# Optimization experiments

Measured on AMD Instinct MI355X. Metric: run time of the kernel, lower is better.

Reference implementation:

```python
import math
import jax, jax.numpy as jnp
import numpy as np

B, L, D = 8, 4096, 1024
H = 8
DK = D // H          # d_keys = d_values = 128
K_FACTOR = 2


def setup_inputs() -> dict:
    key = jax.random.key(0)
    ks = jax.random.split(key, 11)
    s = 0.02
    return {
        "queries": jax.random.normal(ks[0], (B, L, D), dtype=jnp.float32),
        "keys":    jax.random.normal(ks[1], (B, L, D), dtype=jnp.float32),
        "values":  jax.random.normal(ks[2], (B, L, D), dtype=jnp.float32),
        "Wq": jax.random.normal(ks[3], (D, H * DK), dtype=jnp.float32) * s,
        "bq": jnp.zeros((H * DK,), dtype=jnp.float32),
        "Wk": jax.random.normal(ks[4], (D, H * DK), dtype=jnp.float32) * s,
        "bk": jnp.zeros((H * DK,), dtype=jnp.float32),
        "Wv": jax.random.normal(ks[5], (D, H * DK), dtype=jnp.float32) * s,
        "bv": jnp.zeros((H * DK,), dtype=jnp.float32),
        "Wo": jax.random.normal(ks[6], (H * DK, D), dtype=jnp.float32) * s,
        "bo": jnp.zeros((D,), dtype=jnp.float32),
    }


def reference(queries, keys, values, Wq, bq, Wk, bk, Wv, bv, Wo, bo):
    b, l, _ = queries.shape
    # projections + head split: [B, L, H, DK]
    q = (queries @ Wq + bq).reshape(b, l, H, DK)
    k = (keys @ Wk + bk).reshape(b, l, H, DK)
    v = (values @ Wv + bv).reshape(b, l, H, DK)
    # L == S so the pad/truncate branch is a no-op (keys[:, :L] == keys)

    qT = q.transpose(0, 2, 3, 1)  # [B, H, DK, L]
    kT = k.transpose(0, 2, 3, 1)
    vT = v.transpose(0, 2, 3, 1)

    # FFT-based circular cross-correlation along time axis
    q_fft = jnp.fft.rfft(qT, axis=-1)
    k_fft = jnp.fft.rfft(kT, axis=-1)
    corr = jnp.fft.irfft(q_fft * jnp.conj(k_fft), n=l, axis=-1)  # [B, H, DK, L]

    # time-delay aggregation over top-k delays
    top_k = int(K_FACTOR * math.log(l))
    weights, delay = jax.lax.top_k(corr, top_k)        # [B, H, DK, K]
    tmp_corr = jax.nn.softmax(weights, axis=-1)
    tmp_values = jnp.concatenate([vT, vT], axis=-1)    # [B, H, DK, 2L] circular wrap
    init_index = jnp.arange(l)

    delay_k = jnp.moveaxis(delay, -1, 0)               # [K, B, H, DK]
    corr_k = jnp.moveaxis(tmp_corr, -1, 0)             # [K, B, H, DK]

    def step(acc, dc):
        d_i, c_i = dc                                  # [B, H, DK]
        idx = init_index[None, None, None, :] + d_i[..., None]   # [B, H, DK, L]
        pattern = jnp.take_along_axis(tmp_values, idx, axis=-1)
        return acc + pattern * c_i[..., None], None

    agg, _ = jax.lax.scan(step, jnp.zeros_like(vT), (delay_k, corr_k))

    out = agg.transpose(0, 3, 1, 2).reshape(b, l, H * DK)  # [B, L, H*DK]
    return out @ Wo + bo
```

## Files before the change

### kernel.cpp

```cpp
#include <hip/hip_runtime.h>
#include <hip/hip_bf16.h>
#include <string.h>

#define NB 8
#define LSEQ 4096
#define DMOD 1024
#define NCH (NB * DMOD)
#define TOPK 16

typedef unsigned short u16;
typedef unsigned int u32;
typedef __attribute__((ext_vector_type(4))) float f32x4;
typedef __attribute__((ext_vector_type(8))) _Float16 f16x8;

__device__ __forceinline__ float h2f(u16 u) {
  _Float16 h;
  __builtin_memcpy(&h, &u, 2);
  return (float)h;
}
__device__ __forceinline__ u16 f2h(float f) {
  _Float16 h = (_Float16)f;
  u16 u;
  __builtin_memcpy(&u, &h, 2);
  return u;
}
__device__ __forceinline__ u32 pk2(float a, float b) {
  return (u32)f2h(a) | ((u32)f2h(b) << 16);
}

__global__ __launch_bounds__(256) void twiddle_k(float2* tw) {
  int i = blockIdx.x * 256 + threadIdx.x;
  if (i < 2048) {
    float ang = -2.0f * 3.14159265358979323846f * (float)i / 4096.0f;
    tw[i] = make_float2(cosf(ang), sinf(ang));
  }
}

__global__ __launch_bounds__(256) void transpose_w_k(const float* __restrict__ src,
                                                     u16* __restrict__ dst,
                                                     int R, int C) {
  __shared__ u16 tile[64][66];
  int c0 = blockIdx.x * 64, r0 = blockIdx.y * 64;
  int tx = threadIdx.x & 63, ty = threadIdx.x >> 6;
#pragma unroll
  for (int i = 0; i < 16; i++) {
    int r = ty + i * 4;
    tile[r][tx] = f2h(src[(size_t)(r0 + r) * C + c0 + tx]);
  }
  __syncthreads();
#pragma unroll
  for (int i = 0; i < 16; i++) {
    int cc = ty + i * 4;
    dst[(size_t)(c0 + cc) * R + r0 + tx] = tile[tx][cc];
  }
}

__global__ __launch_bounds__(256) void gemm_proj_k(const float* __restrict__ A,
                                                   const u16* __restrict__ Btw,
                                                   const float* __restrict__ bias,
                                                   u16* __restrict__ out,
                                                   int K) {
  __shared__ __align__(16) u16 smem[17408];
  u16* As = smem;
  u16* Bs = smem + 5120;
  int tid = threadIdx.x;
  int lane = tid & 63, wave = tid >> 6;
  int quad = lane >> 4, l15 = lane & 15;
  int m0 = blockIdx.y * 128, n0 = blockIdx.x * 128;
  int wm = (wave >> 1) * 64, wn = (wave & 1) * 64;
  int r_a = tid >> 2, kc = (tid & 3) * 8;

  f32x4 acc[4][4];
#pragma unroll
  for (int i = 0; i < 4; i++)
#pragma unroll
    for (int j = 0; j < 4; j++)
      acc[i][j] = (f32x4){0.f, 0.f, 0.f, 0.f};

  for (int kk = 0; kk < K; kk += 32) {
    __syncthreads();
    const float* ga0 = A + (size_t)(m0 + r_a) * K + kk + kc;
    const float* ga1 = ga0 + (size_t)64 * K;
    float4 x0 = *(const float4*)ga0;
    float4 x1 = *(const float4*)(ga0 + 4);
    float4 y0 = *(const float4*)ga1;
    float4 y1 = *(const float4*)(ga1 + 4);
    uint4 wa, wb;
    wa.x = pk2(x0.x, x0.y); wa.y = pk2(x0.z, x0.w);
    wa.z = pk2(x1.x, x1.y); wa.w = pk2(x1.z, x1.w);
    wb.x = pk2(y0.x, y0.y); wb.y = pk2(y0.z, y0.w);
    wb.z = pk2(y1.x, y1.y); wb.w = pk2(y1.z, y1.w);
    *(uint4*)&As[r_a * 40 + kc] = wa;
    *(uint4*)&As[(r_a + 64) * 40 + kc] = wb;
    const u16* gb = Btw + (size_t)(n0 + r_a) * K + kk + kc;
    *(uint4*)&Bs[r_a * 40 + kc] = *(const uint4*)gb;
    *(uint4*)&Bs[(r_a + 64) * 40 + kc] = *(const uint4*)(gb + (size_t)64 * K);
    __syncthreads();
    f16x8 af[4], bfr[4];
    int ka = quad * 8;
#pragma unroll
    for (int i = 0; i < 4; i++)
      af[i] = *(const f16x8*)&As[(wm + i * 16 + l15) * 40 + ka];
#pragma unroll
    for (int j = 0; j < 4; j++)
      bfr[j] = *(const f16x8*)&Bs[(wn + j * 16 + l15) * 40 + ka];
#pragma unroll
    for (int i = 0; i < 4; i++)
#pragma unroll
      for (int j = 0; j < 4; j++)
        acc[i][j] = __builtin_amdgcn_mfma_f32_16x16x32_f16(af[i], bfr[j], acc[i][j], 0, 0, 0);
  }

  __syncthreads();
  float bv[4];
#pragma unroll
  for (int j = 0; j < 4; j++) bv[j] = bias[n0 + wn + j * 16 + l15];
  u16* Ct = smem;
#pragma unroll
  for (int i = 0; i < 4; i++) {
#pragma unroll
    for (int j = 0; j < 4; j++) {
      int ml = wm + i * 16 + quad * 4;
      int nl = wn + j * 16 + l15;
      unsigned long long pkv = 0;
#pragma unroll
      for (int r = 0; r < 4; r++)
        pkv |= ((unsigned long long)f2h(acc[i][j][r] + bv[j])) << (16 * r);
      *(unsigned long long*)&Ct[nl * 136 + ml] = pkv;
    }
  }
  __syncthreads();
  int b_ = m0 >> 12, t0 = m0 & 4095;
#pragma unroll
  for (int it = 0; it < 8; it++) {
    int row = (tid >> 4) + it * 16;
    int col = (tid & 15) * 8;
    uint4 v = *(const uint4*)&Ct[row * 136 + col];
    *(uint4*)(out + (size_t)b_ * DMOD * LSEQ + (size_t)(n0 + row) * LSEQ + t0 + col) = v;
  }
}

__global__ __launch_bounds__(256) void gemm_tA_k(const u16* __restrict__ Acm,
                                                 const u16* __restrict__ Wot,
                                                 const float* __restrict__ bias,
                                                 float* __restrict__ out) {
  __shared__ __align__(16) u16 smem[17408];
  u32* Ta = (u32*)smem;
  u16* Bs = smem + 4224;
  int tid = threadIdx.x;
  int lane = tid & 63, wave = tid >> 6;
  int quad = lane >> 4, l15 = lane & 15;
  int b = blockIdx.z;
  int m0 = blockIdx.y * 128, n0 = blockIdx.x * 128;
  int wm = (wave >> 1) * 64, wn = (wave & 1) * 64;
  int cp = tid >> 4, t0s = (tid & 15) * 8;
  int r_b = tid >> 2, kc = (tid & 3) * 8;
  const u16* Ab = Acm + (size_t)b * DMOD * LSEQ;

  f32x4 acc[4][4];
#pragma unroll
  for (int i = 0; i < 4; i++)
#pragma unroll
    for (int j = 0; j < 4; j++)
      acc[i][j] = (f32x4){0.f, 0.f, 0.f, 0.f};

  for (int kk = 0; kk < DMOD; kk += 32) {
    __syncthreads();
    const u16* ga = Ab + (size_t)(kk + 2 * cp) * LSEQ + m0 + t0s;
    uint4 v0 = *(const uint4*)ga;
    uint4 v1 = *(const uint4*)(ga + LSEQ);
    int tb = cp * 132 + t0s;
    uint4 w0, w1;
    w0.x = (v0.x & 0xffffu) | (v1.x << 16);
    w0.y = (v0.x >> 16) | (v1.x & 0xffff0000u);
    w0.z = (v0.y & 0xffffu) | (v1.y << 16);
    w0.w = (v0.y >> 16) | (v1.y & 0xffff0000u);
    w1.x = (v0.z & 0xffffu) | (v1.z << 16);
    w1.y = (v0.z >> 16) | (v1.z & 0xffff0000u);
    w1.z = (v0.w & 0xffffu) | (v1.w << 16);
    w1.w = (v0.w >> 16) | (v1.w & 0xffff0000u);
    *(uint4*)&Ta[tb] = w0;
    *(uint4*)&Ta[tb + 4] = w1;
    const u16* gb = Wot + (size_t)(n0 + r_b) * DMOD + kk + kc;
    *(uint4*)&Bs[r_b * 40 + kc] = *(const uint4*)gb;
    *(uint4*)&Bs[(r_b + 64) * 40 + kc] = *(const uint4*)(gb + (size_t)64 * DMOD);
    __syncthreads();
    f16x8 af[4], bfr[4];
    int ka = quad * 8;
#pragma unroll
    for (int i = 0; i < 4; i++) {
      int mrow = wm + i * 16 + l15;
      uint4 fa;
      fa.x = Ta[(quad * 4 + 0) * 132 + mrow];
      fa.y = Ta[(quad * 4 + 1) * 132 + mrow];
      fa.z = Ta[(quad * 4 + 2) * 132 + mrow];
      fa.w = Ta[(quad * 4 + 3) * 132 + mrow];
      af[i] = *(f16x8*)&fa;
    }
#pragma unroll
    for (int j = 0; j < 4; j++)
      bfr[j] = *(const f16x8*)&Bs[(wn + j * 16 + l15) * 40 + ka];
#pragma unroll
    for (int i = 0; i < 4; i++)
#pragma unroll
      for (int j = 0; j < 4; j++)
        acc[i][j] = __builtin_amdgcn_mfma_f32_16x16x32_f16(af[i], bfr[j], acc[i][j], 0, 0, 0);
  }

  float bv[4];
#pragma unroll
  for (int j = 0; j < 4; j++) bv[j] = bias[n0 + wn + j * 16 + l15];
  float* Cf = (float*)smem;
#pragma unroll
  for (int half = 0; half < 2; half++) {
    __syncthreads();
    if ((wave >> 1) == half) {
#pragma unroll
      for (int i = 0; i < 4; i++) {
#pragma unroll
        for (int j = 0; j < 4; j++) {
          int mlocal = i * 16 + quad * 4;
          int nl = wn + j * 16 + l15;
#pragma unroll
          for (int r = 0; r < 4; r++)
            Cf[(mlocal + r) * 132 + nl] = acc[i][j][r] + bv[j];
        }
      }
    }
    __syncthreads();
#pragma unroll
    for (int it = 0; it < 8; it++) {
      int row = (tid >> 5) + it * 8;
      int col = (tid & 31) * 4;
      float4 v = *(const float4*)&Cf[row * 132 + col];
      *(float4*)(out + (size_t)b * LSEQ * DMOD +
                 (size_t)(m0 + half * 64 + row) * DMOD + n0 + col) = v;
    }
  }
}

__global__ __launch_bounds__(256) void fft_corr_topk_k(const u16* __restrict__ Qt,
                                                       const u16* __restrict__ Kt,
                                                       const float2* __restrict__ tw,
                                                       float* __restrict__ topw,
                                                       int* __restrict__ topd) {
  __shared__ float2 buf[2][4096];
  int ch = blockIdx.x;
  int tid = threadIdx.x;
  const u16* qrow = Qt + (size_t)ch * LSEQ;
  const u16* krow = Kt + (size_t)ch * LSEQ;
#pragma unroll
  for (int p = 0; p < 16; p++) {
    int idx = tid + p * 256;
    buf[0][idx] = make_float2(h2f(qrow[idx]), h2f(krow[idx]));
  }
  int srcb = 0, m = 1;
#pragma unroll
  for (int s = 0; s < 12; s++) {
    __syncthreads();
    const float2* src = buf[srcb];
    float2* dst = buf[srcb ^ 1];
#pragma unroll
    for (int p = 0; p < 8; p++) {
      int idx = tid + p * 256;
      int k = idx & (m - 1);
      int jm = idx - k;
      float2 c0 = src[idx];
      float2 c1 = src[idx + 2048];
      float2 w = tw[jm];
      dst[idx + jm] = make_float2(c0.x + c1.x, c0.y + c1.y);
      float2 d = make_float2(c0.x - c1.x, c0.y - c1.y);
      dst[idx + jm + m] = make_float2(d.x * w.x - d.y * w.y, d.x * w.y + d.y * w.x);
    }
    srcb ^= 1;
    m <<= 1;
  }
  __syncthreads();
#pragma unroll
  for (int p = 0; p < 16; p++) {
    int f = tid + p * 256;
    float2 zf = buf[0][f];
    float2 zn = buf[0][(4096 - f) & 4095];
    float2 zc = make_float2(zn.x, -zn.y);
    float2 a = make_float2(zf.x + zc.x, zf.y + zc.y);
    float2 d = make_float2(zf.x - zc.x, zf.y - zc.y);
    float2 dc = make_float2(d.x, -d.y);
    float px = a.x * dc.x - a.y * dc.y;
    float py = a.x * dc.y + a.y * dc.x;
    buf[1][f] = make_float2(-0.25f * py, 0.25f * px);
  }
  srcb = 1; m = 1;
#pragma unroll
  for (int s = 0; s < 12; s++) {
    __syncthreads();
    const float2* src = buf[srcb];
    float2* dst = buf[srcb ^ 1];
#pragma unroll
    for (int p = 0; p < 8; p++) {
      int idx = tid + p * 256;
      int k = idx & (m - 1);
      int jm = idx - k;
      float2 c0 = src[idx];
      float2 c1 = src[idx + 2048];
      float2 w = tw[jm];
      w.y = -w.y;
      dst[idx + jm] = make_float2(c0.x + c1.x, c0.y + c1.y);
      float2 d = make_float2(c0.x - c1.x, c0.y - c1.y);
      dst[idx + jm + m] = make_float2(d.x * w.x - d.y * w.y, d.x * w.y + d.y * w.x);
    }
    srcb ^= 1;
    m <<= 1;
  }
  __syncthreads();
  float* scr = (float*)buf[0];
  float* tv = scr + 8;
  int* tdl = (int*)(scr + 24);
  const float NEGINF = -__builtin_inff();
  for (int r = 0; r < TOPK; r++) {
    float bvv = NEGINF;
    int bi = 0;
    for (int p = 0; p < 16; p++) {
      int t = tid + p * 256;
      float v = buf[1][t].x;
      if (v > bvv) { bvv = v; bi = t; }
    }
#pragma unroll
    for (int off = 32; off > 0; off >>= 1) {
      float ov = __shfl_down(bvv, off);
      int oi = __shfl_down(bi, off);
      if (ov > bvv || (ov == bvv && oi < bi)) { bvv = ov; bi = oi; }
    }
    if ((tid & 63) == 0) { scr[tid >> 6] = bvv; ((int*)scr)[4 + (tid >> 6)] = bi; }
    __syncthreads();
    if (tid == 0) {
      float fb = scr[0]; int fi = ((int*)scr)[4];
      for (int wv = 1; wv < 4; wv++) {
        float ov = scr[wv]; int oi = ((int*)scr)[4 + wv];
        if (ov > fb || (ov == fb && oi < fi)) { fb = ov; fi = oi; }
      }
      tv[r] = fb; tdl[r] = fi;
      buf[1][fi].x = NEGINF;
    }
    __syncthreads();
  }
  if (tid == 0) {
    float mx = tv[0];
    float e[TOPK];
    float s = 0.f;
    for (int k2 = 0; k2 < TOPK; k2++) {
      e[k2] = __expf((tv[k2] - mx) * (1.0f / 4096.0f));
      s += e[k2];
    }
    float inv = 1.0f / s;
    for (int k2 = 0; k2 < TOPK; k2++) {
      topw[(size_t)ch * TOPK + k2] = e[k2] * inv;
      topd[(size_t)ch * TOPK + k2] = tdl[k2];
    }
  }
}

__global__ __launch_bounds__(256) void aggregate_k(const u16* __restrict__ Vt,
                                                   const float* __restrict__ topw,
                                                   const int* __restrict__ topd,
                                                   u16* __restrict__ agg) {
  __shared__ u16 vrow[4096];
  __shared__ float w_s[TOPK];
  __shared__ int d_s[TOPK];
  int ch = blockIdx.x, tid = threadIdx.x;
  const u16* src = Vt + (size_t)ch * LSEQ;
#pragma unroll
  for (int p = 0; p < 16; p++) vrow[tid + p * 256] = src[tid + p * 256];
  if (tid < TOPK) {
    w_s[tid] = topw[(size_t)ch * TOPK + tid];
    d_s[tid] = topd[(size_t)ch * TOPK + tid];
  }
  __syncthreads();
#pragma unroll
  for (int p = 0; p < 16; p++) {
    int t = tid + p * 256;
    float s = 0.f;
#pragma unroll
    for (int k = 0; k < TOPK; k++)
      s += w_s[k] * h2f(vrow[(t + d_s[k]) & 4095]);
    agg[(size_t)ch * LSEQ + t] = f2h(s);
  }
}

extern "C" void kernel_launch(void* const* d_in, const int* in_sizes, int n_in,
                              void* d_out, int out_size, void* d_ws, size_t ws_size,
                              hipStream_t stream) {
  (void)in_sizes; (void)n_in; (void)out_size; (void)ws_size;
  const float* queries = (const float*)d_in[0];
  const float* keys    = (const float*)d_in[1];
  const float* values  = (const float*)d_in[2];
  const float* Wq = (const float*)d_in[3];
  const float* bq = (const float*)d_in[4];
  const float* Wk = (const float*)d_in[5];
  const float* bk = (const float*)d_in[6];
  const float* Wv = (const float*)d_in[7];
  const float* bv = (const float*)d_in[8];
  const float* Wo = (const float*)d_in[9];
  const float* bo = (const float*)d_in[10];

  char* ws = (char*)d_ws;
  u16* ws0 = (u16*)ws;
  u16* Wqt = (u16*)(ws + (64ull << 20));
  u16* Wkt = Wqt + 1024 * 1024;
  u16* Wvt = Wkt + 1024 * 1024;
  u16* Wot = Wvt + 1024 * 1024;
  float2* tw = (float2*)(ws + (72ull << 20));
  float* topw = (float*)(ws + (72ull << 20) + (64ull << 10));
  int* topd = (int*)(ws + (72ull << 20) + (64ull << 10) + (512ull << 10));

  u16* Qt = ws0;
  u16* Kt = (u16*)d_out;
  u16* Vt = (u16*)d_out;
  u16* agg = ws0;

  twiddle_k<<<dim3(8), dim3(256), 0, stream>>>(tw);
  transpose_w_k<<<dim3(16, 16), dim3(256), 0, stream>>>(Wq, Wqt, 1024, 1024);
  transpose_w_k<<<dim3(16, 16), dim3(256), 0, stream>>>(Wk, Wkt, 1024, 1024);
  transpose_w_k<<<dim3(16, 16), dim3(256), 0, stream>>>(Wv, Wvt, 1024, 1024);
  transpose_w_k<<<dim3(16, 16), dim3(256), 0, stream>>>(Wo, Wot, 1024, 1024);
  dim3 gg(8, 256);
  gemm_proj_k<<<gg, dim3(256), 0, stream>>>(queries, Wqt, bq, Qt, 1024);
  gemm_proj_k<<<gg, dim3(256), 0, stream>>>(keys, Wkt, bk, Kt, 1024);
  fft_corr_topk_k<<<dim3(NCH), dim3(256), 0, stream>>>(Qt, Kt, tw, topw, topd);
  gemm_proj_k<<<gg, dim3(256), 0, stream>>>(values, Wvt, bv, Vt, 1024);
  aggregate_k<<<dim3(NCH), dim3(256), 0, stream>>>(Vt, topw, topd, agg);
  gemm_tA_k<<<dim3(8, 32, 8), dim3(256), 0, stream>>>(agg, Wot, bo, (float*)d_out);
}
```

Baseline: 1.588 ms.

## Replace radix-2 Stockham FFT with register radix-16 FFT and incremental top-k

The FFT correlation kernel now runs a three-pass radix-16 decomposition in registers, with swizzled shared-memory exchanges between passes. This replaces 12 radix-2 stages per transform, each with its own barrier and double-buffered shared memory. The twiddle table grows to the full 4096 entries, shared memory drops to a single buffer, and launch bounds ask for 4 blocks per CU. Top-k keeps a per-thread maximum candidate that only the winning thread recomputes each round, instead of rescanning all 4096 values every round. This adds register pressure and more complex indexing.

Measured after the change: 1.461 ms. -8.0%, faster.

```diff
diff --git a/kernel.cpp b/kernel.cpp
--- a/kernel.cpp
+++ b/kernel.cpp
@@ -27,10 +27,16 @@
 __device__ __forceinline__ u32 pk2(float a, float b) {
   return (u32)f2h(a) | ((u32)f2h(b) << 16);
 }
+__device__ __forceinline__ float2 cmul(float2 a, float2 b) {
+  return make_float2(a.x * b.x - a.y * b.y, a.x * b.y + a.y * b.x);
+}
+__device__ __forceinline__ float2 cmul_conj(float2 a, float2 b) {
+  return make_float2(a.x * b.x + a.y * b.y, a.y * b.x - a.x * b.y);
+}
 
 __global__ __launch_bounds__(256) void twiddle_k(float2* tw) {
   int i = blockIdx.x * 256 + threadIdx.x;
-  if (i < 2048) {
+  if (i < 4096) {
     float ang = -2.0f * 3.14159265358979323846f * (float)i / 4096.0f;
     tw[i] = make_float2(cosf(ang), sinf(ang));
   }
@@ -239,122 +245,214 @@
   }
 }
 
-__global__ __launch_bounds__(256) void fft_corr_topk_k(const u16* __restrict__ Qt,
-                                                       const u16* __restrict__ Kt,
-                                                       const float2* __restrict__ tw,
-                                                       float* __restrict__ topw,
-                                                       int* __restrict__ topd) {
-  __shared__ float2 buf[2][4096];
+#define SWZ(t) ((t) ^ (((t) >> 4) & 15))
+
+template <bool INV>
+__device__ __forceinline__ void dft16(float2* z) {
+  const float SQ = 0.70710678118654752440f;
+  const float C1 = 0.92387953251128675613f;
+  const float S1 = 0.38268343236508977173f;
+  const float sg = INV ? 1.0f : -1.0f;
+#pragma unroll
+  for (int i = 0; i < 16; i += 2) {
+    float2 a = z[i], b = z[i + 1];
+    z[i] = make_float2(a.x + b.x, a.y + b.y);
+    z[i + 1] = make_float2(a.x - b.x, a.y - b.y);
+  }
+  {
+    const float wre[2] = {1.f, 0.f};
+    const float wim[2] = {0.f, sg};
+#pragma unroll
+    for (int g = 0; g < 16; g += 4)
+#pragma unroll
+      for (int p = 0; p < 2; p++) {
+        float2 a = z[g + p], b = z[g + p + 2];
+        float2 t = make_float2(b.x * wre[p] - b.y * wim[p],
+                               b.x * wim[p] + b.y * wre[p]);
+        z[g + p] = make_float2(a.x + t.x, a.y + t.y);
+        z[g + p + 2] = make_float2(a.x - t.x, a.y - t.y);
+      }
+  }
+  {
+    const float wre[4] = {1.f, SQ, 0.f, -SQ};
+    const float wim[4] = {0.f, sg * SQ, sg, sg * SQ};
+#pragma unroll
+    for (int g = 0; g < 16; g += 8)
+#pragma unroll
+      for (int p = 0; p < 4; p++) {
+        float2 a = z[g + p], b = z[g + p + 4];
+        float2 t = make_float2(b.x * wre[p] - b.y * wim[p],
+                               b.x * wim[p] + b.y * wre[p]);
+        z[g + p] = make_float2(a.x + t.x, a.y + t.y);
+        z[g + p + 4] = make_float2(a.x - t.x, a.y - t.y);
+      }
+  }
+  {
+    const float wre[8] = {1.f, C1, SQ, S1, 0.f, -S1, -SQ, -C1};
+    const float wim[8] = {0.f, sg * S1, sg * SQ, sg * C1, sg, sg * C1, sg * SQ, sg * S1};
+#pragma unroll
+    for (int p = 0; p < 8; p++) {
+      float2 a = z[p], b = z[p + 8];
+      float2 t = make_float2(b.x * wre[p] - b.y * wim[p],
+                             b.x * wim[p] + b.y * wre[p]);
+      z[p] = make_float2(a.x + t.x, a.y + t.y);
+      z[p + 8] = make_float2(a.x - t.x, a.y - t.y);
+    }
+  }
+}
+
+__global__ __launch_bounds__(256, 4) void fft_corr_topk_k(const u16* __restrict__ Qt,
+                                                          const u16* __restrict__ Kt,
+                                                          const float2* __restrict__ tw,
+                                                          float* __restrict__ topw,
+                                                          int* __restrict__ topd) {
+  __shared__ float2 buf[4096];
+  __shared__ float candv[256];
+  __shared__ int candi[256];
+  __shared__ float tvs[TOPK];
+  __shared__ int tds[TOPK];
+  __shared__ int winner;
   int ch = blockIdx.x;
   int tid = threadIdx.x;
   const u16* qrow = Qt + (size_t)ch * LSEQ;
   const u16* krow = Kt + (size_t)ch * LSEQ;
-#pragma unroll
-  for (int p = 0; p < 16; p++) {
-    int idx = tid + p * 256;
-    buf[0][idx] = make_float2(h2f(qrow[idx]), h2f(krow[idx]));
-  }
-  int srcb = 0, m = 1;
-#pragma unroll
-  for (int s = 0; s < 12; s++) {
-    __syncthreads();
-    const float2* src = buf[srcb];
-    float2* dst = buf[srcb ^ 1];
-#pragma unroll
-    for (int p = 0; p < 8; p++) {
-      int idx = tid + p * 256;
-      int k = idx & (m - 1);
-      int jm = idx - k;
-      float2 c0 = src[idx];
-      float2 c1 = src[idx + 2048];
-      float2 w = tw[jm];
-      dst[idx + jm] = make_float2(c0.x + c1.x, c0.y + c1.y);
-      float2 d = make_float2(c0.x - c1.x, c0.y - c1.y);
-      dst[idx + jm + m] = make_float2(d.x * w.x - d.y * w.y, d.x * w.y + d.y * w.x);
-    }
-    srcb ^= 1;
-    m <<= 1;
-  }
-  __syncthreads();
-#pragma unroll
-  for (int p = 0; p < 16; p++) {
-    int f = tid + p * 256;
-    float2 zf = buf[0][f];
-    float2 zn = buf[0][(4096 - f) & 4095];
-    float2 zc = make_float2(zn.x, -zn.y);
-    float2 a = make_float2(zf.x + zc.x, zf.y + zc.y);
-    float2 d = make_float2(zf.x - zc.x, zf.y - zc.y);
-    float2 dc = make_float2(d.x, -d.y);
-    float px = a.x * dc.x - a.y * dc.y;
-    float py = a.x * dc.y + a.y * dc.x;
-    buf[1][f] = make_float2(-0.25f * py, 0.25f * px);
-  }
-  srcb = 1; m = 1;
-#pragma unroll
-  for (int s = 0; s < 12; s++) {
-    __syncthreads();
-    const float2* src = buf[srcb];
-    float2* dst = buf[srcb ^ 1];
-#pragma unroll
-    for (int p = 0; p < 8; p++) {
-      int idx = tid + p * 256;
-      int k = idx & (m - 1);
-      int jm = idx - k;
-      float2 c0 = src[idx];
-      float2 c1 = src[idx + 2048];
-      float2 w = tw[jm];
-      w.y = -w.y;
-      dst[idx + jm] = make_float2(c0.x + c1.x, c0.y + c1.y);
-      float2 d = make_float2(c0.x - c1.x, c0.y - c1.y);
-      dst[idx + jm + m] = make_float2(d.x * w.x - d.y * w.y, d.x * w.y + d.y * w.x);
-    }
-    srcb ^= 1;
-    m <<= 1;
-  }
-  __syncthreads();
-  float* scr = (float*)buf[0];
-  float* tv = scr + 8;
-  int* tdl = (int*)(scr + 24);
+  const int rev[16] = {0, 8, 4, 12, 2, 10, 6, 14, 1, 9, 5, 13, 3, 11, 7, 15};
+  float2 z[16];
+
+#pragma unroll
+  for (int r = 0; r < 16; r++) {
+    int t = tid + 256 * r;
+    z[rev[r]] = make_float2(h2f(qrow[t]), h2f(krow[t]));
+  }
+  dft16<false>(z);
+#pragma unroll
+  for (int u = 0; u < 16; u++) {
+    float2 w = tw[(u * tid) & 4095];
+    buf[SWZ(16 * tid + u)] = cmul(z[u], w);
+  }
+  __syncthreads();
+
+  {
+    int k16 = tid & 15, j = tid >> 4;
+#pragma unroll
+    for (int r = 0; r < 16; r++) z[rev[r]] = buf[SWZ(tid + 256 * r)];
+    __syncthreads();
+    dft16<false>(z);
+#pragma unroll
+    for (int u = 0; u < 16; u++) {
+      float2 w = tw[(u * j * 16) & 4095];
+      buf[SWZ(256 * j + k16 + 16 * u)] = cmul(z[u], w);
+    }
+  }
+  __syncthreads();
+
+#pragma unroll
+  for (int r = 0; r < 16; r++) z[rev[r]] = buf[SWZ(tid + 256 * r)];
+  __syncthreads();
+  dft16<false>(z);
+#pragma unroll
+  for (int u = 0; u < 16; u++) buf[SWZ(tid + 256 * u)] = z[u];
+  __syncthreads();
+
+#pragma unroll
+  for (int r = 0; r < 16; r++) {
+    int t = tid + 256 * r;
+    float2 zf = buf[SWZ(t)];
+    float2 zn = buf[SWZ((4096 - t) & 4095)];
+    float ax = zf.x + zn.x, ay = zf.y - zn.y;
+    float dx = zf.x - zn.x, dy = zf.y + zn.y;
+    float px = ax * dx + ay * dy;
+    float py = ay * dx - ax * dy;
+    z[rev[r]] = make_float2(-0.25f * py, 0.25f * px);
+  }
+  __syncthreads();
+  dft16<true>(z);
+#pragma unroll
+  for (int u = 0; u < 16; u++) {
+    float2 w = tw[(u * tid) & 4095];
+    buf[SWZ(16 * tid + u)] = cmul_conj(z[u], w);
+  }
+  __syncthreads();
+
+  {
+    int k16 = tid & 15, j = tid >> 4;
+#pragma unroll
+    for (int r = 0; r < 16; r++) z[rev[r]] = buf[SWZ(tid + 256 * r)];
+    __syncthreads();
+    dft16<true>(z);
+#pragma unroll
+    for (int u = 0; u < 16; u++) {
+      float2 w = tw[(u * j * 16) & 4095];
+      buf[SWZ(256 * j + k16 + 16 * u)] = cmul_conj(z[u], w);
+    }
+  }
+  __syncthreads();
+
+#pragma unroll
+  for (int r = 0; r < 16; r++) z[rev[r]] = buf[SWZ(tid + 256 * r)];
+  dft16<true>(z);
+  float vals[16];
+#pragma unroll
+  for (int u = 0; u < 16; u++) vals[u] = z[u].x;
+
   const float NEGINF = -__builtin_inff();
+  {
+    float bvv = vals[0];
+    int bu = 0;
+#pragma unroll
+    for (int u = 1; u < 16; u++)
+      if (vals[u] > bvv) { bvv = vals[u]; bu = u; }
+    candv[tid] = bvv;
+    candi[tid] = tid + (bu << 8);
+  }
   for (int r = 0; r < TOPK; r++) {
-    float bvv = NEGINF;
-    int bi = 0;
-    for (int p = 0; p < 16; p++) {
-      int t = tid + p * 256;
-      float v = buf[1][t].x;
-      if (v > bvv) { bvv = v; bi = t; }
-    }
-#pragma unroll
-    for (int off = 32; off > 0; off >>= 1) {
-      float ov = __shfl_down(bvv, off);
-      int oi = __shfl_down(bi, off);
-      if (ov > bvv || (ov == bvv && oi < bi)) { bvv = ov; bi = oi; }
-    }
-    if ((tid & 63) == 0) { scr[tid >> 6] = bvv; ((int*)scr)[4 + (tid >> 6)] = bi; }
-    __syncthreads();
-    if (tid == 0) {
-      float fb = scr[0]; int fi = ((int*)scr)[4];
-      for (int wv = 1; wv < 4; wv++) {
-        float ov = scr[wv]; int oi = ((int*)scr)[4 + wv];
-        if (ov > fb || (ov == fb && oi < fi)) { fb = ov; fi = oi; }
+    __syncthreads();
+    if (tid < 64) {
+      float v0 = candv[tid];
+      int i0 = candi[tid];
+#pragma unroll
+      for (int s2 = 1; s2 < 4; s2++) {
+        float v1 = candv[tid + 64 * s2];
+        int i1 = candi[tid + 64 * s2];
+        if (v1 > v0 || (v1 == v0 && i1 < i0)) { v0 = v1; i0 = i1; }
       }
-      tv[r] = fb; tdl[r] = fi;
-      buf[1][fi].x = NEGINF;
-    }
-    __syncthreads();
-  }
+#pragma unroll
+      for (int off = 32; off > 0; off >>= 1) {
+        float ov = __shfl_down(v0, off);
+        int oi = __shfl_down(i0, off);
+        if (ov > v0 || (ov == v0 && oi < i0)) { v0 = ov; i0 = oi; }
+      }
+      if (tid == 0) { tvs[r] = v0; tds[r] = i0; winner = i0; }
+    }
+    __syncthreads();
+    int wn = winner;
+    if ((wn & 255) == tid) {
+      int ku = wn >> 8;
+#pragma unroll
+      for (int u = 0; u < 16; u++)
+        if (u == ku) vals[u] = NEGINF;
+      float bvv = vals[0];
+      int bu = 0;
+#pragma unroll
+      for (int u = 1; u < 16; u++)
+        if (vals[u] > bvv) { bvv = vals[u]; bu = u; }
+      candv[tid] = bvv;
+      candi[tid] = tid + (bu << 8);
+    }
+  }
+  __syncthreads();
   if (tid == 0) {
-    float mx = tv[0];
+    float mx = tvs[0];
     float e[TOPK];
     float s = 0.f;
     for (int k2 = 0; k2 < TOPK; k2++) {
-      e[k2] = __expf((tv[k2] - mx) * (1.0f / 4096.0f));
+      e[k2] = __expf((tvs[k2] - mx) * (1.0f / 4096.0f));
       s += e[k2];
     }
     float inv = 1.0f / s;
     for (int k2 = 0; k2 < TOPK; k2++) {
       topw[(size_t)ch * TOPK + k2] = e[k2] * inv;
-      topd[(size_t)ch * TOPK + k2] = tdl[k2];
+      topd[(size_t)ch * TOPK + k2] = tds[k2];
     }
   }
 }
@@ -417,7 +515,7 @@
   u16* Vt = (u16*)d_out;
   u16* agg = ws0;
 
-  twiddle_k<<<dim3(8), dim3(256), 0, stream>>>(tw);
+  twiddle_k<<<dim3(16), dim3(256), 0, stream>>>(tw);
   transpose_w_k<<<dim3(16, 16), dim3(256), 0, stream>>>(Wq, Wqt, 1024, 1024);
   transpose_w_k<<<dim3(16, 16), dim3(256), 0, stream>>>(Wk, Wkt, 1024, 1024);
   transpose_w_k<<<dim3(16, 16), dim3(256), 0, stream>>>(Wv, Wvt, 1024, 1024);
```

## Rewrite FFT correlation as register radix-16 passes with swizzled LDS and incremental top-k

Applied to the files above, without the earlier changes.

Replaces the 12-stage radix-2 Stockham FFT, which did two shared-memory round trips per stage, with a three-pass radix-16 decomposition held in registers. Twiddles are applied between passes and shared memory is XOR-swizzled to avoid bank conflicts. Shared memory drops to one buffer, and launch bounds request four blocks per CU. Top-k selection now keeps a per-thread candidate list and rescans only the winning thread's 16 values each round, instead of rescanning all 4096 with a full block reduction. The twiddle table grows to 4096 entries, and the higher register count per thread may limit occupancy.

Result: faster. 1.439 ms (-9.4%).

```diff
diff --git a/kernel.cpp b/kernel.cpp
--- a/kernel.cpp
+++ b/kernel.cpp
@@ -27,10 +27,16 @@
 __device__ __forceinline__ u32 pk2(float a, float b) {
   return (u32)f2h(a) | ((u32)f2h(b) << 16);
 }
+__device__ __forceinline__ float2 cmul(float2 a, float2 b) {
+  return make_float2(a.x * b.x - a.y * b.y, a.x * b.y + a.y * b.x);
+}
+__device__ __forceinline__ float2 cmul_conj(float2 a, float2 b) {
+  return make_float2(a.x * b.x + a.y * b.y, a.y * b.x - a.x * b.y);
+}
 
 __global__ __launch_bounds__(256) void twiddle_k(float2* tw) {
   int i = blockIdx.x * 256 + threadIdx.x;
-  if (i < 2048) {
+  if (i < 4096) {
     float ang = -2.0f * 3.14159265358979323846f * (float)i / 4096.0f;
     tw[i] = make_float2(cosf(ang), sinf(ang));
   }
@@ -239,122 +245,167 @@
   }
 }
 
-__global__ __launch_bounds__(256) void fft_corr_topk_k(const u16* __restrict__ Qt,
-                                                       const u16* __restrict__ Kt,
-                                                       const float2* __restrict__ tw,
-                                                       float* __restrict__ topw,
-                                                       int* __restrict__ topd) {
-  __shared__ float2 buf[2][4096];
+#define SWZ(t) ((t) ^ (((t) >> 4) & 15))
+
+#define FOREACH16(M) M(0) M(1) M(2) M(3) M(4) M(5) M(6) M(7) \
+                     M(8) M(9) M(10) M(11) M(12) M(13) M(14) M(15)
+#define BITREV16(M) M(0,0) M(1,8) M(2,4) M(3,12) M(4,2) M(5,10) M(6,6) M(7,14) \
+                    M(8,1) M(9,9) M(10,5) M(11,13) M(12,3) M(13,11) M(14,7) M(15,15)
+
+#define BF(a, b) { float tx = (b).x, ty = (b).y; \
+                   (b).x = (a).x - tx; (b).y = (a).y - ty; \
+                   (a).x += tx; (a).y += ty; }
+#define BFW(a, b, wr, wi) { float tx = (b).x*(wr) - (b).y*(wi); \
+                            float ty = (b).x*(wi) + (b).y*(wr); \
+                            (b).x = (a).x - tx; (b).y = (a).y - ty; \
+                            (a).x += tx; (a).y += ty; }
+
+#define FFT_SQ 0.70710678118654752440f
+#define FFT_C1 0.92387953251128675613f
+#define FFT_S1 0.38268343236508977173f
+
+#define DFT16(SGc) \
+  BF(z0,z1) BF(z2,z3) BF(z4,z5) BF(z6,z7) BF(z8,z9) BF(z10,z11) BF(z12,z13) BF(z14,z15) \
+  BF(z0,z2) BFW(z1,z3,0.f,(SGc)) BF(z4,z6) BFW(z5,z7,0.f,(SGc)) \
+  BF(z8,z10) BFW(z9,z11,0.f,(SGc)) BF(z12,z14) BFW(z13,z15,0.f,(SGc)) \
+  BF(z0,z4) BFW(z1,z5,FFT_SQ,(SGc)*FFT_SQ) BFW(z2,z6,0.f,(SGc)) BFW(z3,z7,-FFT_SQ,(SGc)*FFT_SQ) \
+  BF(z8,z12) BFW(z9,z13,FFT_SQ,(SGc)*FFT_SQ) BFW(z10,z14,0.f,(SGc)) BFW(z11,z15,-FFT_SQ,(SGc)*FFT_SQ) \
+  BF(z0,z8) BFW(z1,z9,FFT_C1,(SGc)*FFT_S1) BFW(z2,z10,FFT_SQ,(SGc)*FFT_SQ) BFW(z3,z11,FFT_S1,(SGc)*FFT_C1) \
+  BFW(z4,z12,0.f,(SGc)) BFW(z5,z13,-FFT_S1,(SGc)*FFT_C1) BFW(z6,z14,-FFT_SQ,(SGc)*FFT_SQ) BFW(z7,z15,-FFT_C1,(SGc)*FFT_S1)
+
+__global__ __launch_bounds__(256, 4)
+void fft_corr_topk_k(const u16* __restrict__ Qt,
+                     const u16* __restrict__ Kt,
+                     const float2* __restrict__ tw,
+                     float* __restrict__ topw,
+                     int* __restrict__ topd) {
+  __shared__ float2 buf[4096];
+  __shared__ float candv[256];
+  __shared__ int candi[256];
+  __shared__ float tvs[TOPK];
+  __shared__ int tds[TOPK];
+  __shared__ int winner;
   int ch = blockIdx.x;
   int tid = threadIdx.x;
   const u16* qrow = Qt + (size_t)ch * LSEQ;
   const u16* krow = Kt + (size_t)ch * LSEQ;
-#pragma unroll
-  for (int p = 0; p < 16; p++) {
-    int idx = tid + p * 256;
-    buf[0][idx] = make_float2(h2f(qrow[idx]), h2f(krow[idx]));
-  }
-  int srcb = 0, m = 1;
-#pragma unroll
-  for (int s = 0; s < 12; s++) {
-    __syncthreads();
-    const float2* src = buf[srcb];
-    float2* dst = buf[srcb ^ 1];
-#pragma unroll
-    for (int p = 0; p < 8; p++) {
-      int idx = tid + p * 256;
-      int k = idx & (m - 1);
-      int jm = idx - k;
-      float2 c0 = src[idx];
-      float2 c1 = src[idx + 2048];
-      float2 w = tw[jm];
-      dst[idx + jm] = make_float2(c0.x + c1.x, c0.y + c1.y);
-      float2 d = make_float2(c0.x - c1.x, c0.y - c1.y);
-      dst[idx + jm + m] = make_float2(d.x * w.x - d.y * w.y, d.x * w.y + d.y * w.x);
-    }
-    srcb ^= 1;
-    m <<= 1;
-  }
-  __syncthreads();
-#pragma unroll
-  for (int p = 0; p < 16; p++) {
-    int f = tid + p * 256;
-    float2 zf = buf[0][f];
-    float2 zn = buf[0][(4096 - f) & 4095];
-    float2 zc = make_float2(zn.x, -zn.y);
-    float2 a = make_float2(zf.x + zc.x, zf.y + zc.y);
-    float2 d = make_float2(zf.x - zc.x, zf.y - zc.y);
-    float2 dc = make_float2(d.x, -d.y);
-    float px = a.x * dc.x - a.y * dc.y;
-    float py = a.x * dc.y + a.y * dc.x;
-    buf[1][f] = make_float2(-0.25f * py, 0.25f * px);
-  }
-  srcb = 1; m = 1;
-#pragma unroll
-  for (int s = 0; s < 12; s++) {
-    __syncthreads();
-    const float2* src = buf[srcb];
-    float2* dst = buf[srcb ^ 1];
-#pragma unroll
-    for (int p = 0; p < 8; p++) {
-      int idx = tid + p * 256;
-      int k = idx & (m - 1);
-      int jm = idx - k;
-      float2 c0 = src[idx];
-      float2 c1 = src[idx + 2048];
-      float2 w = tw[jm];
-      w.y = -w.y;
-      dst[idx + jm] = make_float2(c0.x + c1.x, c0.y + c1.y);
-      float2 d = make_float2(c0.x - c1.x, c0.y - c1.y);
-      dst[idx + jm + m] = make_float2(d.x * w.x - d.y * w.y, d.x * w.y + d.y * w.x);
-    }
-    srcb ^= 1;
-    m <<= 1;
-  }
-  __syncthreads();
-  float* scr = (float*)buf[0];
-  float* tv = scr + 8;
-  int* tdl = (int*)(scr + 24);
+  const int jj = tid >> 4, k16 = tid & 15;
+
+#define DECLZ(u) float2 z##u;
+  FOREACH16(DECLZ)
+
+#define LD1(r, k) { int t = tid + 256 * (r); \
+                    z##k = make_float2(h2f(qrow[t]), h2f(krow[t])); }
+  BITREV16(LD1)
+  DFT16(-1.f)
+#define ST1(u) { float2 w = tw[((u) * tid) & 4095]; \
+                 buf[SWZ(16 * tid + (u))] = cmul(z##u, w); }
+  FOREACH16(ST1)
+  __syncthreads();
+
+#define LD2(r, k) z##k = buf[SWZ(tid + 256 * (r))];
+  BITREV16(LD2)
+  __syncthreads();
+  DFT16(-1.f)
+#define ST2F(u) { float2 w = tw[((u) * jj * 16) & 4095]; \
+                  buf[SWZ(256 * jj + k16 + 16 * (u))] = cmul(z##u, w); }
+  FOREACH16(ST2F)
+  __syncthreads();
+
+  BITREV16(LD2)
+  __syncthreads();
+  DFT16(-1.f)
+#define ST3(u) buf[SWZ(tid + 256 * (u))] = z##u;
+  FOREACH16(ST3)
+  __syncthreads();
+
+#define LDP(r, k) { int t = tid + 256 * (r); \
+                    float2 zf = buf[SWZ(t)]; \
+                    float2 zn = buf[SWZ((4096 - t) & 4095)]; \
+                    float ax = zf.x + zn.x, ay = zf.y - zn.y; \
+                    float dx = zf.x - zn.x, dy = zf.y + zn.y; \
+                    float px = ax * dx + ay * dy; \
+                    float py = ay * dx - ax * dy; \
+                    z##k = make_float2(-0.25f * py, 0.25f * px); }
+  BITREV16(LDP)
+  __syncthreads();
+  DFT16(1.f)
+#define ST1I(u) { float2 w = tw[((u) * tid) & 4095]; \
+                  buf[SWZ(16 * tid + (u))] = cmul_conj(z##u, w); }
+  FOREACH16(ST1I)
+  __syncthreads();
+
+  BITREV16(LD2)
+  __syncthreads();
+  DFT16(1.f)
+#define ST2I(u) { float2 w = tw[((u) * jj * 16) & 4095]; \
+                  buf[SWZ(256 * jj + k16 + 16 * (u))] = cmul_conj(z##u, w); }
+  FOREACH16(ST2I)
+  __syncthreads();
+
+  BITREV16(LD2)
+  DFT16(1.f)
+#define DECLV(u) float v##u = z##u.x;
+  FOREACH16(DECLV)
+
   const float NEGINF = -__builtin_inff();
+  {
+    float bvv = v0;
+    int bu = 0;
+#define AMX(u) if (v##u > bvv) { bvv = v##u; bu = (u); }
+    AMX(1) AMX(2) AMX(3) AMX(4) AMX(5) AMX(6) AMX(7)
+    AMX(8) AMX(9) AMX(10) AMX(11) AMX(12) AMX(13) AMX(14) AMX(15)
+    candv[tid] = bvv;
+    candi[tid] = tid + (bu << 8);
+  }
   for (int r = 0; r < TOPK; r++) {
-    float bvv = NEGINF;
-    int bi = 0;
-    for (int p = 0; p < 16; p++) {
-      int t = tid + p * 256;
-      float v = buf[1][t].x;
-      if (v > bvv) { bvv = v; bi = t; }
-    }
-#pragma unroll
-    for (int off = 32; off > 0; off >>= 1) {
-      float ov = __shfl_down(bvv, off);
-      int oi = __shfl_down(bi, off);
-      if (ov > bvv || (ov == bvv && oi < bi)) { bvv = ov; bi = oi; }
-    }
-    if ((tid & 63) == 0) { scr[tid >> 6] = bvv; ((int*)scr)[4 + (tid >> 6)] = bi; }
-    __syncthreads();
-    if (tid == 0) {
-      float fb = scr[0]; int fi = ((int*)scr)[4];
-      for (int wv = 1; wv < 4; wv++) {
-        float ov = scr[wv]; int oi = ((int*)scr)[4 + wv];
-        if (ov > fb || (ov == fb && oi < fi)) { fb = ov; fi = oi; }
+    __syncthreads();
+    if (tid < 64) {
+      float v0r = candv[tid];
+      int i0r = candi[tid];
+#pragma unroll
+      for (int s2 = 1; s2 < 4; s2++) {
+        float v1r = candv[tid + 64 * s2];
+        int i1r = candi[tid + 64 * s2];
+        if (v1r > v0r || (v1r == v0r && i1r < i0r)) { v0r = v1r; i0r = i1r; }
       }
-      tv[r] = fb; tdl[r] = fi;
-      buf[1][fi].x = NEGINF;
-    }
-    __syncthreads();
-  }
+#pragma unroll
+      for (int off = 32; off > 0; off >>= 1) {
+        float ov = __shfl_down(v0r, off);
+        int oi = __shfl_down(i0r, off);
+        if (ov > v0r || (ov == v0r && oi < i0r)) { v0r = ov; i0r = oi; }
+      }
+      if (tid == 0) { tvs[r] = v0r; tds[r] = i0r; winner = i0r; }
+    }
+    __syncthreads();
+    int wnr = winner;
+    if ((wnr & 255) == tid) {
+      int ku = wnr >> 8;
+#define KILLV(u) if (ku == (u)) v##u = NEGINF;
+      FOREACH16(KILLV)
+      float bvv = v0;
+      int bu = 0;
+      AMX(1) AMX(2) AMX(3) AMX(4) AMX(5) AMX(6) AMX(7)
+      AMX(8) AMX(9) AMX(10) AMX(11) AMX(12) AMX(13) AMX(14) AMX(15)
+      candv[tid] = bvv;
+      candi[tid] = tid + (bu << 8);
+    }
+  }
+  __syncthreads();
   if (tid == 0) {
-    float mx = tv[0];
+    float mx = tvs[0];
     float e[TOPK];
     float s = 0.f;
+#pragma unroll
     for (int k2 = 0; k2 < TOPK; k2++) {
-      e[k2] = __expf((tv[k2] - mx) * (1.0f / 4096.0f));
+      e[k2] = __expf((tvs[k2] - mx) * (1.0f / 4096.0f));
       s += e[k2];
     }
     float inv = 1.0f / s;
+#pragma unroll
     for (int k2 = 0; k2 < TOPK; k2++) {
       topw[(size_t)ch * TOPK + k2] = e[k2] * inv;
-      topd[(size_t)ch * TOPK + k2] = tdl[k2];
+      topd[(size_t)ch * TOPK + k2] = tds[k2];
     }
   }
 }
@@ -417,7 +468,7 @@
   u16* Vt = (u16*)d_out;
   u16* agg = ws0;
 
-  twiddle_k<<<dim3(8), dim3(256), 0, stream>>>(tw);
+  twiddle_k<<<dim3(16), dim3(256), 0, stream>>>(tw);
   transpose_w_k<<<dim3(16, 16), dim3(256), 0, stream>>>(Wq, Wqt, 1024, 1024);
   transpose_w_k<<<dim3(16, 16), dim3(256), 0, stream>>>(Wk, Wkt, 1024, 1024);
   transpose_w_k<<<dim3(16, 16), dim3(256), 0, stream>>>(Wv, Wvt, 1024, 1024);
```
